# Kernel tuning notes

Measured on AMD Instinct MI355X. Metric: run time of the kernel, lower is better.

## Reference

```python
import jax, jax.numpy as jnp
import numpy as np

EPS = 0.01       # perturbation radius (constructor arg)
MEAN = 0.1307    # MNIST normalize constants from the 'else' branch
SIGMA = 0.3081


def _get_bound(v, eps):
    # torch get_bound detaches eps before taking |.| and summing
    r = jnp.sum(jnp.abs(jax.lax.stop_gradient(eps)), axis=-1)
    return v + r, v - r


def _relu_zono(v, eps):
    # v: [N], eps: [N, E]. Append one fresh (zero) error column, as the torch code does.
    n = v.shape[0]
    eps = jnp.concatenate([eps, jnp.zeros((n, 1), eps.dtype)], axis=-1)  # [N, E+1]
    u, l = _get_bound(v, eps)
    denom = u - l  # = 2*sum|eps| >= 0; guard against 0 for non-crossing rows
    # slopes are created as Parameters = u/(u-l) on the first pass (detached leaf)
    slope = jax.lax.stop_gradient(u / jnp.where(denom == 0, 1.0, denom))
    # at init slope == base = u/(u-l), so the slope <= base branch is taken
    term = (1.0 - slope) * u * 0.5
    crossing = (u > 0) & (l < 0)
    dead = u <= 0
    # torch uses slope.data * values.data for the linear part, + term (term carries grad)
    v_cross = jax.lax.stop_gradient(slope * v) + term
    v_new = jnp.where(dead, 0.0, jnp.where(crossing, v_cross, v))
    eps_cross = jnp.concatenate([slope[:, None] * eps[:, :-1], term[:, None]], axis=-1)
    eps_new = jnp.where(dead[:, None], 0.0, jnp.where(crossing[:, None], eps_cross, eps))
    return v_new, eps_new


def _forward(inputs, W1, b1, W2, b2, W3, b3):
    # initial zonotope build (faithful to source: values = u + l, radii = values - l = u)
    upper = jnp.minimum(inputs + EPS, 1.0)   # upper - relu(upper - 1)
    lower = jnp.maximum(inputs - EPS, 0.0)   # relu(lower)
    values = upper + lower
    eps = jnp.diag((values - lower).flatten())  # [D, D]
    # Normalize layer (the 'else' branch)
    values = (values - MEAN) / SIGMA
    eps = eps / SIGMA
    # Flatten
    v = values.flatten()
    # Linear -> ReLU -> Linear -> ReLU -> Linear
    v = W1 @ v + b1
    eps = W1 @ eps
    v, eps = _relu_zono(v, eps)
    v = W2 @ v + b2
    eps = W2 @ eps
    v, eps = _relu_zono(v, eps)
    v = W3 @ v + b3
    eps = W3 @ eps
    u, l = _get_bound(v, eps)
    return u, l


def setup_inputs() -> dict:
    key = jax.random.key(0)
    ks = jax.random.split(key, 7)
    D, H, O = 1024, 4096, 10
    inputs = jax.random.uniform(ks[0], (1, 1, 32, 32), jnp.float32)
    W1 = jax.random.normal(ks[1], (H, D), jnp.float32) / np.float32(np.sqrt(D))
    b1 = jax.random.normal(ks[2], (H,), jnp.float32) * 0.01
    W2 = jax.random.normal(ks[3], (H, H), jnp.float32) / np.float32(np.sqrt(H))
    b2 = jax.random.normal(ks[4], (H,), jnp.float32) * 0.01
    W3 = jax.random.normal(ks[5], (O, H), jnp.float32) / np.float32(np.sqrt(H))
    b3 = jax.random.normal(ks[6], (O,), jnp.float32) * 0.01
    return {"inputs": inputs, "W1": W1, "b1": b1, "W2": W2, "b2": b2, "W3": W3, "b3": b3}


def reference(inputs, W1, b1, W2, b2, W3, b3):
    return _forward(inputs, W1, b1, W2, b2, W3, b3)
```

## Files before the change

kernel.cpp:

```cpp
#include <hip/hip_runtime.h>
#include <math.h>

#define ZEPS  0.01f
#define ZMEAN 0.1307f
#define ZSIGMA 0.3081f

constexpr int D = 1024, H = 4096, O = 10;

using short8 = __attribute__((ext_vector_type(8))) short;
using f32x4  = __attribute__((ext_vector_type(4))) float;

__device__ inline unsigned short f2bf(float x) {
    unsigned int u = __float_as_uint(x);
    u += 0x7FFFu + ((u >> 16) & 1u);
    return (unsigned short)(u >> 16);
}

__device__ inline unsigned int f2bf2_fast(float a, float b) {
    unsigned int ua = __float_as_uint(a) + 0x8000u;
    unsigned int ub = __float_as_uint(b) + 0x8000u;
    return (ua >> 16) | (ub & 0xFFFF0000u);
}

__device__ inline void gl_lds16(const void* g, void* l) {
    __builtin_amdgcn_global_load_lds(
        (const __attribute__((address_space(1))) unsigned int*)g,
        (__attribute__((address_space(3))) unsigned int*)l, 16, 0, 0);
}

__device__ inline float zval(float xv) {
    float up = fminf(xv + ZEPS, 1.f);
    float lo = fmaxf(xv - ZEPS, 0.f);
    return (up + lo - ZMEAN) / ZSIGMA;
}
__device__ inline float zdia(float xv) {
    return fminf(xv + ZEPS, 1.f) / ZSIGMA;
}

__device__ inline void relu_params(float v, float r, float& vout, float& aout, float& tout) {
    float u = v + r, l = v - r;
    float denom = u - l;
    float slope = u / (denom == 0.f ? 1.f : denom);
    float term = (1.f - slope) * u * 0.5f;
    bool dead = (u <= 0.f);
    bool crossing = (u > 0.f) && (l < 0.f);
    vout = dead ? 0.f : (crossing ? (slope * v + term) : v);
    aout = dead ? 0.f : (crossing ? slope : 1.f);
    tout = (!dead && crossing) ? term : 0.f;
}

__global__ __launch_bounds__(256) void k_layer1(const float* __restrict__ W1, const float* __restrict__ b1,
                                                const float* __restrict__ x,
                                                float* __restrict__ v1p, float* __restrict__ a1,
                                                float* __restrict__ t1) {
    int wid = threadIdx.x >> 6, lane = threadIdx.x & 63;
    int i = blockIdx.x * 4 + wid;
    const float* row = W1 + (size_t)i * D;
    float sv = 0.f, sr = 0.f;
#pragma unroll
    for (int it = 0; it < 4; ++it) {
        int j = it * 256 + lane * 4;
        float4 w = *(const float4*)&row[j];
        float4 xx = *(const float4*)&x[j];
        sv += w.x * zval(xx.x) + w.y * zval(xx.y) + w.z * zval(xx.z) + w.w * zval(xx.w);
        sr += fabsf(w.x) * zdia(xx.x) + fabsf(w.y) * zdia(xx.y) +
              fabsf(w.z) * zdia(xx.z) + fabsf(w.w) * zdia(xx.w);
    }
#pragma unroll
    for (int m = 1; m <= 32; m <<= 1) {
        sv += __shfl_xor(sv, m, 64);
        sr += __shfl_xor(sr, m, 64);
    }
    if (lane == 0) {
        float vo, ao, to;
        relu_params(sv + b1[i], sr, vo, ao, to);
        v1p[i] = vo; a1[i] = ao; t1[i] = to;
    }
}

__global__ __launch_bounds__(256) void k_scaleT(const float* __restrict__ W1, const float* __restrict__ a1,
                                                const float* __restrict__ x,
                                                unsigned short* __restrict__ W1sT) {
    __shared__ float tile[32][33];
    int j0 = blockIdx.x * 32, k0 = blockIdx.y * 32;
    int r = threadIdx.x >> 3;
    int c = (threadIdx.x & 7) * 4;
    float4 w = *(const float4*)&W1[(size_t)(k0 + r) * D + j0 + c];
    float4 xx = *(const float4*)&x[j0 + c];
    float a = a1[k0 + r];
    tile[r][c + 0] = a * w.x * zdia(xx.x);
    tile[r][c + 1] = a * w.y * zdia(xx.y);
    tile[r][c + 2] = a * w.z * zdia(xx.z);
    tile[r][c + 3] = a * w.w * zdia(xx.w);
    __syncthreads();
    ushort4 o;
    o.x = f2bf(tile[c + 0][r]);
    o.y = f2bf(tile[c + 1][r]);
    o.z = f2bf(tile[c + 2][r]);
    o.w = f2bf(tile[c + 3][r]);
    *(ushort4*)&W1sT[(size_t)(j0 + r) * H + k0 + c] = o;
}

#define GBK 64
__global__ __launch_bounds__(256) void k_gemm_mfma(const float* __restrict__ A,
                                                   const unsigned short* __restrict__ B,
                                                   const float* __restrict__ v1p,
                                                   const float* __restrict__ t1,
                                                   float* __restrict__ C,
                                                   float* __restrict__ vpart,
                                                   float* __restrict__ tpart) {
    const int N = D, K = H;
    __shared__ __align__(16) unsigned short As[128 * GBK];
    __shared__ __align__(16) unsigned short Bs[128 * GBK];
    __shared__ float vt[2048], tt[2048];
    int b = blockIdx.x;
    int u = b & 7, v = b >> 3;
    int z = u >> 2;
    int y = (u & 3) * 8 + (v >> 3);
    int xb = v & 7;
    int tid = threadIdx.x;
    int wave = tid >> 6, lane = tid & 63;
    int bm = y * 128, bn = xb * 128;
    int kbeg = z * (K / 2);
    float* Cz = C + (size_t)z * ((size_t)H * D);
    int wm = (wave >> 1) * 64, wn = (wave & 1) * 64;

    int srow = lane >> 3, sc = lane & 7, scp = sc ^ srow;
    int r15 = lane & 15, quad = lane >> 4, key = r15 & 7;
    int rowg = tid >> 3, ch = tid & 7;
    int aswz = ch ^ (rowg & 7);

    for (int idx = tid; idx < 512; idx += 256) {
        *(float4*)&vt[idx * 4] = *(const float4*)&v1p[kbeg + idx * 4];
        *(float4*)&tt[idx * 4] = *(const float4*)&t1[kbeg + idx * 4];
    }
    __syncthreads();

    f32x4 acc[4][4];
#pragma unroll
    for (int p = 0; p < 4; ++p)
#pragma unroll
        for (int q = 0; q < 4; ++q) acc[p][q] = (f32x4){0.f, 0.f, 0.f, 0.f};
    float sv[4] = {0.f, 0.f, 0.f, 0.f}, st[4] = {0.f, 0.f, 0.f, 0.f};

    for (int s = 0; s < (K / 2) / GBK; ++s) {
        int k0 = kbeg + s * GBK;
#pragma unroll
        for (int g = 0; g < 4; ++g) {
            int row = wave * 32 + g * 8;
            gl_lds16(&B[(size_t)(bn + row + srow) * K + k0 + scp * 8], &Bs[row * GBK]);
        }
        bool dodot = ((s & 7) == xb);
#pragma unroll
        for (int g = 0; g < 4; ++g) {
            int row = g * 32 + rowg;
            const float* ap = &A[(size_t)(bm + row) * K + k0 + ch * 8];
            float4 a0 = *(const float4*)ap;
            float4 a1v = *(const float4*)(ap + 4);
            if (dodot) {
                const float* vp = &vt[s * 64 + ch * 8];
                const float* tp = &tt[s * 64 + ch * 8];
                float4 v0 = *(const float4*)vp, v1 = *(const float4*)(vp + 4);
                float4 t0 = *(const float4*)tp, t1v = *(const float4*)(tp + 4);
                sv[g] += a0.x * v0.x + a0.y * v0.y + a0.z * v0.z + a0.w * v0.w
                       + a1v.x * v1.x + a1v.y * v1.y + a1v.z * v1.z + a1v.w * v1.w;
                st[g] += a0.x * t0.x + a0.y * t0.y + a0.z * t0.z + a0.w * t0.w
                       + a1v.x * t1v.x + a1v.y * t1v.y + a1v.z * t1v.z + a1v.w * t1v.w;
            }
            uint4 hh;
            hh.x = f2bf2_fast(a0.x, a0.y);
            hh.y = f2bf2_fast(a0.z, a0.w);
            hh.z = f2bf2_fast(a1v.x, a1v.y);
            hh.w = f2bf2_fast(a1v.z, a1v.w);
            *(uint4*)&As[row * GBK + aswz * 8] = hh;
        }
        __syncthreads();
#pragma unroll
        for (int kk = 0; kk < 2; ++kk) {
            short8 af[4], bf[4];
#pragma unroll
            for (int mt = 0; mt < 4; ++mt)
                af[mt] = *(const short8*)&As[(wm + mt * 16 + r15) * GBK + (((kk * 4 + quad) ^ key)) * 8];
#pragma unroll
            for (int nt = 0; nt < 4; ++nt)
                bf[nt] = *(const short8*)&Bs[(wn + nt * 16 + r15) * GBK + (((kk * 4 + quad) ^ key)) * 8];
#pragma unroll
            for (int mt = 0; mt < 4; ++mt)
#pragma unroll
                for (int nt = 0; nt < 4; ++nt)
                    acc[mt][nt] = __builtin_amdgcn_mfma_f32_16x16x32_bf16(af[mt], bf[nt], acc[mt][nt], 0, 0, 0);
        }
        __syncthreads();
    }

#pragma unroll
    for (int mt = 0; mt < 4; ++mt) {
        int gr = bm + wm + mt * 16 + quad * 4;
#pragma unroll
        for (int nt = 0; nt < 4; ++nt) {
            int gc = bn + wn + nt * 16 + r15;
            Cz[(size_t)(gr + 0) * N + gc] = acc[mt][nt][0];
            Cz[(size_t)(gr + 1) * N + gc] = acc[mt][nt][1];
            Cz[(size_t)(gr + 2) * N + gc] = acc[mt][nt][2];
            Cz[(size_t)(gr + 3) * N + gc] = acc[mt][nt][3];
        }
    }

#pragma unroll
    for (int g = 0; g < 4; ++g) {
        float a = sv[g], bb = st[g];
        a += __shfl_xor(a, 1, 64); a += __shfl_xor(a, 2, 64); a += __shfl_xor(a, 4, 64);
        bb += __shfl_xor(bb, 1, 64); bb += __shfl_xor(bb, 2, 64); bb += __shfl_xor(bb, 4, 64);
        if (ch == 0) {
            int i = bm + g * 32 + rowg;
            vpart[(size_t)(z * 8 + xb) * H + i] = a;
            tpart[(size_t)(z * 8 + xb) * H + i] = bb;
        }
    }
}

__global__ __launch_bounds__(256) void k_relu2(const float* __restrict__ e1, const float* __restrict__ e2,
                                               const float* __restrict__ vpart, const float* __restrict__ tpart,
                                               const float* __restrict__ b2, const float* __restrict__ W3,
                                               float* __restrict__ v2p, float* __restrict__ a2,
                                               float* __restrict__ t2, float* __restrict__ t2col,
                                               float* __restrict__ w3s) {
    int wid = threadIdx.x >> 6, lane = threadIdx.x & 63;
    int i = blockIdx.x * 4 + wid;
    float s = 0.f;
#pragma unroll
    for (int it = 0; it < 4; ++it) {
        int j = it * 256 + lane * 4;
        float4 a = *(const float4*)&e1[(size_t)i * D + j];
        float4 b = *(const float4*)&e2[(size_t)i * D + j];
        s += fabsf(a.x + b.x) + fabsf(a.y + b.y) + fabsf(a.z + b.z) + fabsf(a.w + b.w);
    }
    float ve = (lane < 16) ? vpart[(size_t)lane * H + i] : 0.f;
    float te = (lane < 16) ? tpart[(size_t)lane * H + i] : 0.f;
#pragma unroll
    for (int m = 1; m <= 32; m <<= 1) {
        s += __shfl_xor(s, m, 64);
        ve += __shfl_xor(ve, m, 64);
        te += __shfl_xor(te, m, 64);
    }
    float vo, ao, to;
    relu_params(ve + b2[i], s + fabsf(te), vo, ao, to);
    if (lane == 0) { v2p[i] = vo; a2[i] = ao; t2[i] = to; t2col[i] = te; }
    if (lane < O) w3s[(size_t)i * O + lane] = W3[(size_t)lane * H + i] * ao;
}

__global__ __launch_bounds__(256) void k_eps3a(const float* __restrict__ e1, const float* __restrict__ e2,
                                               const float* __restrict__ w3s,
                                               float* __restrict__ pbuf) {
    int jb = blockIdx.x, ib = blockIdx.y;
    int jj = threadIdx.x & 15, s = threadIdx.x >> 4;
    int j = jb * 64 + jj * 4;
    int i0 = ib * 128 + s * 8;
    float acc[4][O];
#pragma unroll
    for (int c = 0; c < 4; ++c)
#pragma unroll
        for (int o = 0; o < O; ++o) acc[c][o] = 0.f;
    for (int ii = 0; ii < 8; ++ii) {
        int i = i0 + ii;
        float4 a = *(const float4*)&e1[(size_t)i * D + j];
        float4 b = *(const float4*)&e2[(size_t)i * D + j];
        float e0 = a.x + b.x, ee1 = a.y + b.y, ee2 = a.z + b.z, ee3 = a.w + b.w;
        const float* w = &w3s[(size_t)i * O];
#pragma unroll
        for (int o = 0; o < O; ++o) {
            float wo = w[o];
            acc[0][o] += wo * e0; acc[1][o] += wo * ee1;
            acc[2][o] += wo * ee2; acc[3][o] += wo * ee3;
        }
    }
    __shared__ float sm[16][64][O];
#pragma unroll
    for (int c = 0; c < 4; ++c)
#pragma unroll
        for (int o = 0; o < O; ++o) sm[s][jj * 4 + c][o] = acc[c][o];
    __syncthreads();
    for (int idx = threadIdx.x; idx < 64 * O; idx += 256) {
        int col = idx / O, o = idx % O;
        float t = 0.f;
#pragma unroll
        for (int ss = 0; ss < 16; ++ss) t += sm[ss][col][o];
        pbuf[((size_t)o * 32 + ib) * D + jb * 64 + col] = t;
    }
}

__global__ __launch_bounds__(256) void k_final(const float* __restrict__ W3, const float* __restrict__ b3,
                                               const float* __restrict__ v2p, const float* __restrict__ a2,
                                               const float* __restrict__ t2col, const float* __restrict__ t2,
                                               const float* __restrict__ pbuf, float* __restrict__ out) {
    int o = blockIdx.x, tid = threadIdx.x;
    float s3 = 0.f;
    for (int j = tid; j < D; j += 256) {
        float t = 0.f;
#pragma unroll
        for (int ib = 0; ib < 32; ++ib) t += pbuf[((size_t)o * 32 + ib) * D + j];
        s3 += fabsf(t);
    }
    const float* row = W3 + (size_t)o * H;
    float sv = 0.f, s1 = 0.f, s2 = 0.f;
    for (int i = tid; i < H; i += 256) {
        float w = row[i];
        sv += w * v2p[i];
        s1 += w * a2[i] * t2col[i];
        s2 += w * t2[i];
    }
    __shared__ float ra[256], rb[256], rc[256], rd[256];
    ra[tid] = sv; rb[tid] = s1; rc[tid] = s2; rd[tid] = s3;
    __syncthreads();
    for (int off = 128; off; off >>= 1) {
        if (tid < off) {
            ra[tid] += ra[tid + off]; rb[tid] += rb[tid + off];
            rc[tid] += rc[tid + off]; rd[tid] += rd[tid + off];
        }
        __syncthreads();
    }
    if (tid == 0) {
        float v3 = ra[0] + b3[o];
        float rr = rd[0] + fabsf(rb[0]) + fabsf(rc[0]);
        out[o] = v3 + rr;
        out[O + o] = v3 - rr;
    }
}

extern "C" void kernel_launch(void* const* d_in, const int* in_sizes, int n_in,
                              void* d_out, int out_size, void* d_ws, size_t ws_size,
                              hipStream_t stream) {
    const float* x  = (const float*)d_in[0];
    const float* W1 = (const float*)d_in[1];
    const float* b1 = (const float*)d_in[2];
    const float* W2 = (const float*)d_in[3];
    const float* b2 = (const float*)d_in[4];
    const float* W3 = (const float*)d_in[5];
    const float* b3 = (const float*)d_in[6];
    float* out = (float*)d_out;

    float* p = (float*)d_ws;
    float* v1p    = p; p += H;
    float* a1     = p; p += H;
    float* t1     = p; p += H;
    float* t2col  = p; p += H;
    float* v2p    = p; p += H;
    float* a2     = p; p += H;
    float* t2     = p; p += H;
    float* w3s    = p; p += H * O + 8;
    float* vpart  = p; p += 16 * H;
    float* tpart  = p; p += 16 * H;
    float* pbuf   = p; p += 32 * O * D;
    float* eps2   = p; p += (size_t)2 * H * D;
    unsigned short* W1sT = (unsigned short*)p;
    float* eps2b = eps2 + (size_t)H * D;

    k_layer1<<<H / 4, 256, 0, stream>>>(W1, b1, x, v1p, a1, t1);
    k_scaleT<<<dim3(D / 32, H / 32), 256, 0, stream>>>(W1, a1, x, W1sT);
    k_gemm_mfma<<<512, 256, 0, stream>>>(W2, W1sT, v1p, t1, eps2, vpart, tpart);
    k_relu2<<<H / 4, 256, 0, stream>>>(eps2, eps2b, vpart, tpart, b2, W3, v2p, a2, t2, t2col, w3s);
    k_eps3a<<<dim3(D / 64, 32), 256, 0, stream>>>(eps2, eps2b, w3s, pbuf);
    k_final<<<O, 256, 0, stream>>>(W3, b3, v2p, a2, t2col, t2, pbuf, out);
}
```

Baseline: 230.1 us.

## Double-buffer GEMM LDS tiles and store split-K eps2 partials in bf16

The MFMA GEMM now uses two LDS buffers, loading and converting the next K-slice of W2 and W1sT while the current slice runs on the matrix cores, so global latency is hidden behind compute. Separately, the two split-K partial eps2 matrices are written as bf16 instead of fp32, which halves the write traffic and the reads in k_relu2 and k_eps3a. In exchange the kernel uses more LDS and registers, and the partial sums are rounded to bf16 before they are combined, which adds error to the bounds.

```diff
diff --git a/kernel.cpp b/kernel.cpp
--- a/kernel.cpp
+++ b/kernel.cpp
@@ -9,11 +9,15 @@
 
 using short8 = __attribute__((ext_vector_type(8))) short;
 using f32x4  = __attribute__((ext_vector_type(4))) float;
+typedef unsigned short ushort_t;
 
 __device__ inline unsigned short f2bf(float x) {
     unsigned int u = __float_as_uint(x);
     u += 0x7FFFu + ((u >> 16) & 1u);
     return (unsigned short)(u >> 16);
+}
+__device__ inline float bf2f(unsigned short h) {
+    return __uint_as_float(((unsigned int)h) << 16);
 }
 
 __device__ inline unsigned int f2bf2_fast(float a, float b) {
@@ -80,7 +84,7 @@
 
 __global__ __launch_bounds__(256) void k_scaleT(const float* __restrict__ W1, const float* __restrict__ a1,
                                                 const float* __restrict__ x,
-                                                unsigned short* __restrict__ W1sT) {
+                                                ushort_t* __restrict__ W1sT) {
     __shared__ float tile[32][33];
     int j0 = blockIdx.x * 32, k0 = blockIdx.y * 32;
     int r = threadIdx.x >> 3;
@@ -103,15 +107,15 @@
 
 #define GBK 64
 __global__ __launch_bounds__(256) void k_gemm_mfma(const float* __restrict__ A,
-                                                   const unsigned short* __restrict__ B,
+                                                   const ushort_t* __restrict__ B,
                                                    const float* __restrict__ v1p,
                                                    const float* __restrict__ t1,
-                                                   float* __restrict__ C,
+                                                   ushort_t* __restrict__ C,
                                                    float* __restrict__ vpart,
                                                    float* __restrict__ tpart) {
     const int N = D, K = H;
-    __shared__ __align__(16) unsigned short As[128 * GBK];
-    __shared__ __align__(16) unsigned short Bs[128 * GBK];
+    __shared__ __align__(16) ushort_t As[2][128 * GBK];
+    __shared__ __align__(16) ushort_t Bs[2][128 * GBK];
     __shared__ float vt[2048], tt[2048];
     int b = blockIdx.x;
     int u = b & 7, v = b >> 3;
@@ -122,7 +126,7 @@
     int wave = tid >> 6, lane = tid & 63;
     int bm = y * 128, bn = xb * 128;
     int kbeg = z * (K / 2);
-    float* Cz = C + (size_t)z * ((size_t)H * D);
+    ushort_t* Cz = C + (size_t)z * ((size_t)H * D);
     int wm = (wave >> 1) * 64, wn = (wave & 1) * 64;
 
     int srow = lane >> 3, sc = lane & 7, scp = sc ^ srow;
@@ -130,66 +134,94 @@
     int rowg = tid >> 3, ch = tid & 7;
     int aswz = ch ^ (rowg & 7);
 
+    const int S = (K / 2) / GBK;
+
+    float4 pa[4][2];
+    float sv[4] = {0.f, 0.f, 0.f, 0.f}, st[4] = {0.f, 0.f, 0.f, 0.f};
+
+    auto issueA = [&](int s) {
+#pragma unroll
+        for (int g = 0; g < 4; ++g) {
+            const float* ap = &A[(size_t)(bm + g * 32 + rowg) * K + kbeg + s * GBK + ch * 8];
+            pa[g][0] = *(const float4*)ap;
+            pa[g][1] = *(const float4*)(ap + 4);
+        }
+    };
+    auto issueB = [&](int s, int buf) {
+#pragma unroll
+        for (int g = 0; g < 2; ++g) {
+            int row = wave * 32 + g * 16;
+            (void)row;
+        }
+#pragma unroll
+        for (int g = 0; g < 4; ++g) {
+            int row = wave * 32 + g * 8;
+            gl_lds16(&B[(size_t)(bn + row + srow) * K + kbeg + s * GBK + scp * 8], &Bs[buf][row * GBK]);
+        }
+    };
+    auto cvtwrite = [&](int s, int buf) {
+        if ((s & 7) == xb) {
+            const float* vp = &vt[s * 64 + ch * 8];
+            const float* tp = &tt[s * 64 + ch * 8];
+            float4 v0 = *(const float4*)vp, v1 = *(const float4*)(vp + 4);
+            float4 t0 = *(const float4*)tp, t1v = *(const float4*)(tp + 4);
+#pragma unroll
+            for (int g = 0; g < 4; ++g) {
+                sv[g] += pa[g][0].x * v0.x + pa[g][0].y * v0.y + pa[g][0].z * v0.z + pa[g][0].w * v0.w
+                       + pa[g][1].x * v1.x + pa[g][1].y * v1.y + pa[g][1].z * v1.z + pa[g][1].w * v1.w;
+                st[g] += pa[g][0].x * t0.x + pa[g][0].y * t0.y + pa[g][0].z * t0.z + pa[g][0].w * t0.w
+                       + pa[g][1].x * t1v.x + pa[g][1].y * t1v.y + pa[g][1].z * t1v.z + pa[g][1].w * t1v.w;
+            }
+        }
+#pragma unroll
+        for (int g = 0; g < 4; ++g) {
+            uint4 hh;
+            hh.x = f2bf2_fast(pa[g][0].x, pa[g][0].y);
+            hh.y = f2bf2_fast(pa[g][0].z, pa[g][0].w);
+            hh.z = f2bf2_fast(pa[g][1].x, pa[g][1].y);
+            hh.w = f2bf2_fast(pa[g][1].z, pa[g][1].w);
+            *(uint4*)&As[buf][(g * 32 + rowg) * GBK + aswz * 8] = hh;
+        }
+    };
+
+    f32x4 acc[4][4];
+#pragma unroll
+    for (int p = 0; p < 4; ++p)
+#pragma unroll
+        for (int q = 0; q < 4; ++q) acc[p][q] = (f32x4){0.f, 0.f, 0.f, 0.f};
+
+    issueA(0);
+    issueB(0, 0);
     for (int idx = tid; idx < 512; idx += 256) {
         *(float4*)&vt[idx * 4] = *(const float4*)&v1p[kbeg + idx * 4];
         *(float4*)&tt[idx * 4] = *(const float4*)&t1[kbeg + idx * 4];
     }
     __syncthreads();
-
-    f32x4 acc[4][4];
-#pragma unroll
-    for (int p = 0; p < 4; ++p)
-#pragma unroll
-        for (int q = 0; q < 4; ++q) acc[p][q] = (f32x4){0.f, 0.f, 0.f, 0.f};
-    float sv[4] = {0.f, 0.f, 0.f, 0.f}, st[4] = {0.f, 0.f, 0.f, 0.f};
-
-    for (int s = 0; s < (K / 2) / GBK; ++s) {
-        int k0 = kbeg + s * GBK;
-#pragma unroll
-        for (int g = 0; g < 4; ++g) {
-            int row = wave * 32 + g * 8;
-            gl_lds16(&B[(size_t)(bn + row + srow) * K + k0 + scp * 8], &Bs[row * GBK]);
-        }
-        bool dodot = ((s & 7) == xb);
-#pragma unroll
-        for (int g = 0; g < 4; ++g) {
-            int row = g * 32 + rowg;
-            const float* ap = &A[(size_t)(bm + row) * K + k0 + ch * 8];
-            float4 a0 = *(const float4*)ap;
-            float4 a1v = *(const float4*)(ap + 4);
-            if (dodot) {
-                const float* vp = &vt[s * 64 + ch * 8];
-                const float* tp = &tt[s * 64 + ch * 8];
-                float4 v0 = *(const float4*)vp, v1 = *(const float4*)(vp + 4);
-                float4 t0 = *(const float4*)tp, t1v = *(const float4*)(tp + 4);
-                sv[g] += a0.x * v0.x + a0.y * v0.y + a0.z * v0.z + a0.w * v0.w
-                       + a1v.x * v1.x + a1v.y * v1.y + a1v.z * v1.z + a1v.w * v1.w;
-                st[g] += a0.x * t0.x + a0.y * t0.y + a0.z * t0.z + a0.w * t0.w
-                       + a1v.x * t1v.x + a1v.y * t1v.y + a1v.z * t1v.z + a1v.w * t1v.w;
-            }
-            uint4 hh;
-            hh.x = f2bf2_fast(a0.x, a0.y);
-            hh.y = f2bf2_fast(a0.z, a0.w);
-            hh.z = f2bf2_fast(a1v.x, a1v.y);
-            hh.w = f2bf2_fast(a1v.z, a1v.w);
-            *(uint4*)&As[row * GBK + aswz * 8] = hh;
-        }
-        __syncthreads();
+    cvtwrite(0, 0);
+    __syncthreads();
+
+    for (int s = 0; s < S; ++s) {
+        int buf = s & 1, nbuf = buf ^ 1;
+        if (s + 1 < S) {
+            issueA(s + 1);
+            issueB(s + 1, nbuf);
+        }
 #pragma unroll
         for (int kk = 0; kk < 2; ++kk) {
             short8 af[4], bf[4];
 #pragma unroll
             for (int mt = 0; mt < 4; ++mt)
-                af[mt] = *(const short8*)&As[(wm + mt * 16 + r15) * GBK + (((kk * 4 + quad) ^ key)) * 8];
+                af[mt] = *(const short8*)&As[buf][(wm + mt * 16 + r15) * GBK + (((kk * 4 + quad) ^ key)) * 8];
 #pragma unroll
             for (int nt = 0; nt < 4; ++nt)
-                bf[nt] = *(const short8*)&Bs[(wn + nt * 16 + r15) * GBK + (((kk * 4 + quad) ^ key)) * 8];
+                bf[nt] = *(const short8*)&Bs[buf][(wn + nt * 16 + r15) * GBK + (((kk * 4 + quad) ^ key)) * 8];
 #pragma unroll
             for (int mt = 0; mt < 4; ++mt)
 #pragma unroll
                 for (int nt = 0; nt < 4; ++nt)
                     acc[mt][nt] = __builtin_amdgcn_mfma_f32_16x16x32_bf16(af[mt], bf[nt], acc[mt][nt], 0, 0, 0);
         }
+        if (s + 1 < S) cvtwrite(s + 1, nbuf);
         __syncthreads();
     }
 
@@ -199,10 +231,10 @@
 #pragma unroll
         for (int nt = 0; nt < 4; ++nt) {
             int gc = bn + wn + nt * 16 + r15;
-            Cz[(size_t)(gr + 0) * N + gc] = acc[mt][nt][0];
-            Cz[(size_t)(gr + 1) * N + gc] = acc[mt][nt][1];
-            Cz[(size_t)(gr + 2) * N + gc] = acc[mt][nt][2];
-            Cz[(size_t)(gr + 3) * N + gc] = acc[mt][nt][3];
+            Cz[(size_t)(gr + 0) * N + gc] = f2bf(acc[mt][nt][0]);
+            Cz[(size_t)(gr + 1) * N + gc] = f2bf(acc[mt][nt][1]);
+            Cz[(size_t)(gr + 2) * N + gc] = f2bf(acc[mt][nt][2]);
+            Cz[(size_t)(gr + 3) * N + gc] = f2bf(acc[mt][nt][3]);
         }
     }
 
@@ -219,7 +251,7 @@
     }
 }
 
-__global__ __launch_bounds__(256) void k_relu2(const float* __restrict__ e1, const float* __restrict__ e2,
+__global__ __launch_bounds__(256) void k_relu2(const ushort_t* __restrict__ e1, const ushort_t* __restrict__ e2,
                                                const float* __restrict__ vpart, const float* __restrict__ tpart,
                                                const float* __restrict__ b2, const float* __restrict__ W3,
                                                float* __restrict__ v2p, float* __restrict__ a2,
@@ -229,11 +261,16 @@
     int i = blockIdx.x * 4 + wid;
     float s = 0.f;
 #pragma unroll
-    for (int it = 0; it < 4; ++it) {
-        int j = it * 256 + lane * 4;
-        float4 a = *(const float4*)&e1[(size_t)i * D + j];
-        float4 b = *(const float4*)&e2[(size_t)i * D + j];
-        s += fabsf(a.x + b.x) + fabsf(a.y + b.y) + fabsf(a.z + b.z) + fabsf(a.w + b.w);
+    for (int it = 0; it < 2; ++it) {
+        int j = lane * 8 + it * 512;
+        ushort4 a0 = *(const ushort4*)&e1[(size_t)i * D + j];
+        ushort4 a1v = *(const ushort4*)&e1[(size_t)i * D + j + 4];
+        ushort4 b0 = *(const ushort4*)&e2[(size_t)i * D + j];
+        ushort4 b1v = *(const ushort4*)&e2[(size_t)i * D + j + 4];
+        s += fabsf(bf2f(a0.x) + bf2f(b0.x)) + fabsf(bf2f(a0.y) + bf2f(b0.y))
+           + fabsf(bf2f(a0.z) + bf2f(b0.z)) + fabsf(bf2f(a0.w) + bf2f(b0.w))
+           + fabsf(bf2f(a1v.x) + bf2f(b1v.x)) + fabsf(bf2f(a1v.y) + bf2f(b1v.y))
+           + fabsf(bf2f(a1v.z) + bf2f(b1v.z)) + fabsf(bf2f(a1v.w) + bf2f(b1v.w));
     }
     float ve = (lane < 16) ? vpart[(size_t)lane * H + i] : 0.f;
     float te = (lane < 16) ? tpart[(size_t)lane * H + i] : 0.f;
@@ -249,7 +286,7 @@
     if (lane < O) w3s[(size_t)i * O + lane] = W3[(size_t)lane * H + i] * ao;
 }
 
-__global__ __launch_bounds__(256) void k_eps3a(const float* __restrict__ e1, const float* __restrict__ e2,
+__global__ __launch_bounds__(256) void k_eps3a(const ushort_t* __restrict__ e1, const ushort_t* __restrict__ e2,
                                                const float* __restrict__ w3s,
                                                float* __restrict__ pbuf) {
     int jb = blockIdx.x, ib = blockIdx.y;
@@ -263,9 +300,10 @@
         for (int o = 0; o < O; ++o) acc[c][o] = 0.f;
     for (int ii = 0; ii < 8; ++ii) {
         int i = i0 + ii;
-        float4 a = *(const float4*)&e1[(size_t)i * D + j];
-        float4 b = *(const float4*)&e2[(size_t)i * D + j];
-        float e0 = a.x + b.x, ee1 = a.y + b.y, ee2 = a.z + b.z, ee3 = a.w + b.w;
+        ushort4 a = *(const ushort4*)&e1[(size_t)i * D + j];
+        ushort4 b = *(const ushort4*)&e2[(size_t)i * D + j];
+        float e0 = bf2f(a.x) + bf2f(b.x), ee1 = bf2f(a.y) + bf2f(b.y);
+        float ee2 = bf2f(a.z) + bf2f(b.z), ee3 = bf2f(a.w) + bf2f(b.w);
         const float* w = &w3s[(size_t)i * O];
 #pragma unroll
         for (int o = 0; o < O; ++o) {
@@ -351,9 +389,9 @@
     float* vpart  = p; p += 16 * H;
     float* tpart  = p; p += 16 * H;
     float* pbuf   = p; p += 32 * O * D;
-    float* eps2   = p; p += (size_t)2 * H * D;
-    unsigned short* W1sT = (unsigned short*)p;
-    float* eps2b = eps2 + (size_t)H * D;
+    ushort_t* eps2  = (ushort_t*)p;
+    ushort_t* W1sT  = eps2 + (size_t)2 * H * D;
+    ushort_t* eps2b = eps2 + (size_t)H * D;
 
     k_layer1<<<H / 4, 256, 0, stream>>>(W1, b1, x, v1p, a1, t1);
     k_scaleT<<<dim3(D / 32, H / 32), 256, 0, stream>>>(W1, a1, x, W1sT);
```

Result: faster. 207.0 us (-10.0%).
